# Optimization experiments

Measured on AMD Instinct MI355X. Metric: run time of the kernel, lower is better.

## Reference

```python
import jax, jax.numpy as jnp
import numpy as np

N_WAY = 5
NKPTS = 17
EMBED = 512
N_SUPPORT = 25  # 5-way 5-shot
N_QUERY = 65536


def setup_inputs() -> dict:
    key = jax.random.key(0)
    ks = jax.random.split(key, 12)
    def lin(k, fan_in, fan_out):
        return jax.random.normal(k, (fan_in, fan_out), jnp.float32) / np.float32(np.sqrt(fan_in))
    return {
        'support_features': jax.random.normal(ks[0], (1, N_SUPPORT, EMBED), jnp.float32),
        'support_keypoints': jax.random.uniform(ks[1], (N_SUPPORT, NKPTS, 2), jnp.float32),
        'query_features': jax.random.normal(ks[2], (N_QUERY, EMBED), jnp.float32),
        'image_coords': jax.random.uniform(ks[3], (N_QUERY, 2), jnp.float32) * 512.0,
        'W1': lin(ks[4], EMBED, EMBED), 'b1': jnp.zeros((EMBED,), jnp.float32),
        'W2': lin(ks[5], EMBED, EMBED), 'b2': jnp.zeros((EMBED,), jnp.float32),
        'Wo1': lin(ks[6], EMBED, EMBED // 2), 'bo1': jnp.zeros((EMBED // 2,), jnp.float32),
        'Wo2': lin(ks[7], EMBED // 2, 2), 'bo2': jnp.zeros((2,), jnp.float32),
        'Wc1': lin(ks[8], EMBED, EMBED // 2), 'bc1': jnp.zeros((EMBED // 2,), jnp.float32),
        'Wc2': lin(ks[9], EMBED // 2, 1), 'bc2': jnp.zeros((1,), jnp.float32),
        'temperature': jnp.float32(1.0),
    }


def reference(support_features, support_keypoints, query_features, image_coords,
              W1, b1, W2, b2, Wo1, bo1, Wo2, bo2, Wc1, bc1, Wc2, bc2, temperature):
    eps = 1e-8
    nkpts = support_keypoints.shape[1]
    n_query = query_features.shape[0]
    D = query_features.shape[-1]

    # --- compute_prototypes (batch_size == 1; per-kpt prototype identical by construction) ---
    sf = support_features.reshape(-1, D)                      # [Ns, D]
    h = jnp.maximum(sf @ W1 + b1, 0.0) @ W2 + b2              # prototype_net MLP
    n_per = h.shape[0] // N_WAY
    proto_way = h.reshape(N_WAY, n_per, D).mean(axis=1)       # [n_way, D]
    prototypes = jnp.broadcast_to(proto_way[:, None, :], (N_WAY, nkpts, D))

    # --- compute_distances: 1 - cosine_sim, scaled by temperature ---
    qn = jnp.linalg.norm(query_features, axis=-1)             # [Nq]
    pn = jnp.linalg.norm(proto_way, axis=-1)                  # [n_way]
    sim = (query_features @ proto_way.T) / jnp.maximum(qn[:, None] * pn[None, :], eps)
    dist_way = (1.0 - sim) / temperature                      # [Nq, n_way]
    distances = jnp.broadcast_to(dist_way[:, :, None], (n_query, N_WAY, nkpts))

    # --- predict_keypoints ---
    # avg over kpts is a no-op (identical per kpt); argmin over ways
    class_predictions = jnp.argmin(dist_way, axis=1)          # [Nq] int
    # softmax over a single scalar == 1.0, so keypoints == offset broadcast over kpts
    offset = jnp.maximum(query_features @ Wo1 + bo1, 0.0) @ Wo2 + bo2   # [Nq, 2]
    conf = jax.nn.sigmoid(jnp.maximum(query_features @ Wc1 + bc1, 0.0) @ Wc2 + bc2)  # [Nq, 1]
    keypoints = jnp.broadcast_to(offset[:, None, :], (n_query, nkpts, 2))
    keypoints = jax.nn.sigmoid(keypoints) * image_coords[:, None, :]    # image_coords provided
    confidence = jnp.broadcast_to(conf, (n_query, nkpts))

    return keypoints, confidence, distances, class_predictions, prototypes
```

## Files before the change

kernel.cpp:

```cpp
#include <hip/hip_runtime.h>
#include <hip/hip_bf16.h>

#define NQ 65536
#define DIM 512
#define HID 256
#define NWAY 5
#define NKPTS 17

typedef short bf16x8 __attribute__((ext_vector_type(8)));
typedef float f32x4 __attribute__((ext_vector_type(4)));
typedef _Float16 half8 __attribute__((ext_vector_type(8)));

static __device__ __forceinline__ unsigned short f2bf(float f) {
    unsigned int x = __float_as_uint(f);
    unsigned int r = (x + 0x7fffu + ((x >> 16) & 1u)) >> 16;
    return (unsigned short)r;
}

static __device__ __forceinline__ void async16(void* l, const void* g) {
    __builtin_amdgcn_global_load_lds(
        (const __attribute__((address_space(1))) unsigned int*)g,
        (__attribute__((address_space(3))) unsigned int*)l, 16, 0, 0);
}

__global__ __launch_bounds__(256) void k_sup(const float* __restrict__ sf,
                                             const float* __restrict__ W1, const float* __restrict__ b1,
                                             float* __restrict__ ws_h1) {
    __shared__ float sfl[512];
    __shared__ float red[4][64];
    int bx = blockIdx.x;
    int s = bx >> 3, cb = bx & 7;
    int t = threadIdx.x;
    if (t < 128) ((float4*)sfl)[t] = ((const float4*)(sf + s * DIM))[t];
    __syncthreads();
    int c = cb * 64 + (t & 63);
    int qd = t >> 6;
    const float* Wp = W1 + (size_t)qd * 128 * DIM + c;
    float acc = 0.0f;
    #pragma unroll 4
    for (int kk = 0; kk < 128; kk++)
        acc += sfl[qd * 128 + kk] * Wp[(size_t)kk * DIM];
    red[qd][t & 63] = acc;
    __syncthreads();
    if (t < 64) {
        float h = red[0][t] + red[1][t] + red[2][t] + red[3][t] + b1[cb * 64 + t];
        ws_h1[s * DIM + cb * 64 + t] = fmaxf(h, 0.0f);
    }
}

__global__ __launch_bounds__(256) void k_mid2(const float* __restrict__ ws_h1,
                                              const float* __restrict__ W2, const float* __restrict__ b2,
                                              const float* __restrict__ Wo1, const float* __restrict__ Wc1,
                                              float* __restrict__ ws_proto, unsigned short* __restrict__ wb) {
    int bx = blockIdx.x;
    int t = threadIdx.x;
    if (bx < 40) {
        __shared__ float ml[512];
        __shared__ float red[4][64];
        int w = bx >> 3, cb = bx & 7;
        for (int i = t; i < 512; i += 256) {
            float sum = 0.0f;
            #pragma unroll
            for (int s5 = 0; s5 < 5; s5++) sum += ws_h1[(w * 5 + s5) * DIM + i];
            ml[i] = sum * 0.2f;
        }
        __syncthreads();
        int c = cb * 64 + (t & 63);
        int qd = t >> 6;
        const float* Wp = W2 + (size_t)qd * 128 * DIM + c;
        float acc = 0.0f;
        #pragma unroll 4
        for (int kk = 0; kk < 128; kk++)
            acc += ml[qd * 128 + kk] * Wp[(size_t)kk * DIM];
        red[qd][t & 63] = acc;
        __syncthreads();
        if (t < 64)
            ws_proto[w * DIM + cb * 64 + t] =
                red[0][t] + red[1][t] + red[2][t] + red[3][t] + b2[cb * 64 + t];
    } else {
        __shared__ unsigned short T[64][72];
        int tb = bx - 40;
        const float* src = (tb < 32) ? Wo1 : Wc1;
        int cofs = (tb < 32) ? 0 : 256;
        int tt = tb & 31;
        int kt = tt >> 2;
        int ct = tt & 3;
        int i = t >> 2;
        int qd = t & 3;
        const float* rp = src + (size_t)(kt * 64 + i) * HID + ct * 64 + qd * 16;
        #pragma unroll
        for (int v = 0; v < 4; v++) {
            float4 x = *(const float4*)(rp + v * 4);
            T[qd * 16 + v * 4 + 0][i] = f2bf(x.x);
            T[qd * 16 + v * 4 + 1][i] = f2bf(x.y);
            T[qd * 16 + v * 4 + 2][i] = f2bf(x.z);
            T[qd * 16 + v * 4 + 3][i] = f2bf(x.w);
        }
        __syncthreads();
        int j = t >> 2;
        int part = t & 3;
        uint4 o0 = *(const uint4*)&T[j][part * 16];
        uint4 o1 = *(const uint4*)&T[j][part * 16 + 8];
        unsigned short* dst = wb + (size_t)(cofs + ct * 64 + j) * DIM + kt * 64 + part * 16;
        *(uint4*)dst = o0;
        *(uint4*)(dst + 8) = o1;
    }
}

__global__ __launch_bounds__(256) void k_dist(const float* __restrict__ qf,
                                              const float* __restrict__ ws_proto,
                                              const float* __restrict__ temp_p,
                                              float* __restrict__ out_dist, float* __restrict__ out_class,
                                              float* __restrict__ out_proto) {
    __shared__ float pn_lds[8];
    __shared__ float dlds[64 * NWAY];
    int bx = blockIdx.x, t = threadIdx.x;
    int wv = t >> 6, lane = t & 63;

    if (bx < NWAY * NKPTS && t < 128) {
        f32x4 v = *(const f32x4*)(ws_proto + (bx / NKPTS) * DIM + t * 4);
        *(f32x4*)(out_proto + (size_t)bx * DIM + t * 4) = v;
    }
    for (int w = wv; w < NWAY; w += 4) {
        f32x4 a = *(const f32x4*)(ws_proto + w * DIM + lane * 8);
        f32x4 b = *(const f32x4*)(ws_proto + w * DIM + lane * 8 + 4);
        float ss = a[0]*a[0] + a[1]*a[1] + a[2]*a[2] + a[3]*a[3]
                 + b[0]*b[0] + b[1]*b[1] + b[2]*b[2] + b[3]*b[3];
        #pragma unroll
        for (int off = 32; off > 0; off >>= 1) ss += __shfl_xor(ss, off, 64);
        if (lane == 0) pn_lds[w] = sqrtf(ss);
    }
    float invt = 1.0f / temp_p[0];
    __syncthreads();

    int q = bx * 64 + wv * 16 + (lane & 15);
    int kq = (lane >> 4) * 128;
    const float* qp = qf + (size_t)q * DIM + kq;
    const float* pp = ws_proto + kq;

    float ds[NWAY] = {0, 0, 0, 0, 0};
    float qq = 0.0f;
    #pragma unroll 4
    for (int c = 0; c < 16; c++) {
        f32x4 v0 = *(const f32x4*)(qp + c * 8);
        f32x4 v1 = *(const f32x4*)(qp + c * 8 + 4);
        qq += v0[0]*v0[0] + v0[1]*v0[1] + v0[2]*v0[2] + v0[3]*v0[3]
            + v1[0]*v1[0] + v1[1]*v1[1] + v1[2]*v1[2] + v1[3]*v1[3];
        #pragma unroll
        for (int w = 0; w < NWAY; w++) {
            f32x4 p0 = *(const f32x4*)(pp + w * DIM + c * 8);
            f32x4 p1 = *(const f32x4*)(pp + w * DIM + c * 8 + 4);
            ds[w] += v0[0]*p0[0] + v0[1]*p0[1] + v0[2]*p0[2] + v0[3]*p0[3]
                   + v1[0]*p1[0] + v1[1]*p1[1] + v1[2]*p1[2] + v1[3]*p1[3];
        }
    }
    #pragma unroll
    for (int off = 16; off <= 32; off <<= 1) {
        #pragma unroll
        for (int w = 0; w < NWAY; w++) ds[w] += __shfl_xor(ds[w], off, 64);
        qq += __shfl_xor(qq, off, 64);
    }
    if (lane < 16) {
        float qn = sqrtf(qq);
        float mv = 1e30f; int ami = 0;
        #pragma unroll
        for (int w = 0; w < NWAY; w++) {
            float den = fmaxf(qn * pn_lds[w], 1e-8f);
            float d = (1.0f - ds[w] / den) * invt;
            dlds[(wv * 16 + lane) * NWAY + w] = d;
            if (d < mv) { mv = d; ami = w; }
        }
        out_class[q] = (float)ami;
    }
    __syncthreads();
    int Q0 = bx * 64;
    for (int i = t; i < 64 * NWAY * NKPTS; i += 256) {
        int q2 = i / (NWAY * NKPTS);
        int rem = i - q2 * (NWAY * NKPTS);
        out_dist[(size_t)(Q0 + q2) * (NWAY * NKPTS) + rem] = dlds[q2 * NWAY + rem / NKPTS];
    }
}

__global__ __launch_bounds__(256, 3) void k_gemm(const float* __restrict__ qf,
                                                 const unsigned short* __restrict__ wb,
                                                 const float* __restrict__ bo1, const float* __restrict__ Wo2,
                                                 const float* __restrict__ bo2,
                                                 const float* __restrict__ bc1, const float* __restrict__ Wc2,
                                                 const float* __restrict__ bc2,
                                                 const float* __restrict__ ic,
                                                 float* __restrict__ out_kp, float* __restrict__ out_conf) {
    __shared__ __align__(16) char smem[40960];
    char* Ab = smem;
    char* Bb = smem + 8192;
    _Float16* hl = (_Float16*)smem;
    float* redf = (float*)(smem + 33792);

    int bx = blockIdx.x;
    int mb = bx & 1023, nb = bx >> 10;
    int t = threadIdx.x;
    int wv = t >> 6, lane = t & 63;
    int r = lane & 15, hq = lane >> 4;

    int am = t >> 2, akc = t & 3;
    const float* Ag = qf + ((size_t)mb * 64 + am) * DIM + akc * 8;
    int awoff = am * 64 + ((akc ^ (am & 3) ^ ((am >> 2) & 1)) << 4);

    int srow = lane >> 2;
    int sg = (lane & 3) ^ (srow & 3) ^ ((srow >> 2) & 1);
    const unsigned short* Bg = wb + (size_t)(nb * 256 + wv * 64 + srow) * DIM + sg * 8;

    f32x4 acc[4][4];
    #pragma unroll
    for (int i2 = 0; i2 < 4; i2++)
        #pragma unroll
        for (int j2 = 0; j2 < 4; j2++) { f32x4 z = {0.0f, 0.0f, 0.0f, 0.0f}; acc[i2][j2] = z; }

    float4 aW0 = *(const float4*)(Ag);
    float4 aW1 = *(const float4*)(Ag + 4);
    #pragma unroll
    for (int i = 0; i < 4; i++)
        async16(Bb + wv * 4096 + i * 1024, Bg + (size_t)i * 16 * DIM);
    float4 aN0 = *(const float4*)(Ag + 32);
    float4 aN1 = *(const float4*)(Ag + 36);
    {
        unsigned int p0 = f2bf(aW0.x) | ((unsigned int)f2bf(aW0.y) << 16);
        unsigned int p1 = f2bf(aW0.z) | ((unsigned int)f2bf(aW0.w) << 16);
        unsigned int p2 = f2bf(aW1.x) | ((unsigned int)f2bf(aW1.y) << 16);
        unsigned int p3 = f2bf(aW1.z) | ((unsigned int)f2bf(aW1.w) << 16);
        *(uint4*)(Ab + awoff) = make_uint4(p0, p1, p2, p3);
    }
    aW0 = aN0; aW1 = aN1;
    asm volatile("s_waitcnt lgkmcnt(0) vmcnt(2)" ::: "memory");
    __builtin_amdgcn_s_barrier();
    __builtin_amdgcn_sched_barrier(0);

    int slot8 = (hq ^ (r & 3) ^ ((r >> 2) & 1)) * 8;

    for (int it = 0; it < 15; it++) {
        int par = it & 1;
        #pragma unroll
        for (int i = 0; i < 4; i++)
            async16(Bb + (par ^ 1) * 16384 + wv * 4096 + i * 1024,
                    Bg + (size_t)i * 16 * DIM + (it + 1) * 32);
        float4 aL0, aL1;
        if (it < 14) {
            aL0 = *(const float4*)(Ag + (it + 2) * 32);
            aL1 = *(const float4*)(Ag + (it + 2) * 32 + 4);
        }
        {
            unsigned int p0 = f2bf(aW0.x) | ((unsigned int)f2bf(aW0.y) << 16);
            unsigned int p1 = f2bf(aW0.z) | ((unsigned int)f2bf(aW0.w) << 16);
            unsigned int p2 = f2bf(aW1.x) | ((unsigned int)f2bf(aW1.y) << 16);
            unsigned int p3 = f2bf(aW1.z) | ((unsigned int)f2bf(aW1.w) << 16);
            *(uint4*)(Ab + (par ^ 1) * 4096 + awoff) = make_uint4(p0, p1, p2, p3);
        }
        const unsigned short* Ap = (const unsigned short*)(Ab + par * 4096);
        const unsigned short* Bp = (const unsigned short*)(Bb + par * 16384);
        bf16x8 af[4], bfr[4];
        #pragma unroll
        for (int mt = 0; mt < 4; mt++)
            af[mt] = *(const bf16x8*)(Ap + (mt * 16 + r) * 32 + slot8);
        #pragma unroll
        for (int nt = 0; nt < 4; nt++)
            bfr[nt] = *(const bf16x8*)(Bp + (wv * 64 + nt * 16 + r) * 32 + slot8);
        #pragma unroll
        for (int mt = 0; mt < 4; mt++)
            #pragma unroll
            for (int nt = 0; nt < 4; nt++)
                acc[mt][nt] = __builtin_amdgcn_mfma_f32_16x16x32_bf16(af[mt], bfr[nt], acc[mt][nt], 0, 0, 0);
        if (it < 14) { asm volatile("s_waitcnt lgkmcnt(0) vmcnt(2)" ::: "memory"); }
        else         { asm volatile("s_waitcnt lgkmcnt(0) vmcnt(0)" ::: "memory"); }
        __builtin_amdgcn_s_barrier();
        __builtin_amdgcn_sched_barrier(0);
        if (it < 14) { aW0 = aL0; aW1 = aL1; }
    }
    {
        const unsigned short* Ap = (const unsigned short*)(Ab + 4096);
        const unsigned short* Bp = (const unsigned short*)(Bb + 16384);
        bf16x8 af[4], bfr[4];
        #pragma unroll
        for (int mt = 0; mt < 4; mt++)
            af[mt] = *(const bf16x8*)(Ap + (mt * 16 + r) * 32 + slot8);
        #pragma unroll
        for (int nt = 0; nt < 4; nt++)
            bfr[nt] = *(const bf16x8*)(Bp + (wv * 64 + nt * 16 + r) * 32 + slot8);
        #pragma unroll
        for (int mt = 0; mt < 4; mt++)
            #pragma unroll
            for (int nt = 0; nt < 4; nt++)
                acc[mt][nt] = __builtin_amdgcn_mfma_f32_16x16x32_bf16(af[mt], bfr[nt], acc[mt][nt], 0, 0, 0);
    }
    __syncthreads();

    const float* bias = nb ? bc1 : bo1;
    #pragma unroll
    for (int nt = 0; nt < 4; nt++) {
        int cl = wv * 64 + nt * 16 + r;
        float bv = bias[cl];
        #pragma unroll
        for (int mt = 0; mt < 4; mt++)
            #pragma unroll
            for (int rg = 0; rg < 4; rg++) {
                int ml = mt * 16 + hq * 4 + rg;
                hl[ml * 264 + cl] = (_Float16)fmaxf(acc[mt][nt][rg] + bv, 0.0f);
            }
    }
    __syncthreads();

    int q = t & 63, qt = t >> 6;
    if (nb == 0) {
        float ox = 0.0f, oy = 0.0f;
        #pragma unroll 2
        for (int j0 = 0; j0 < 64; j0 += 8) {
            half8 hv = *(const half8*)(hl + q * 264 + qt * 64 + j0);
            #pragma unroll
            for (int j = 0; j < 8; j++) {
                float2 w2 = *(const float2*)(Wo2 + (qt * 64 + j0 + j) * 2);
                float hf = (float)hv[j];
                ox += hf * w2.x;
                oy += hf * w2.y;
            }
        }
        redf[(qt * 64 + q) * 2] = ox;
        redf[(qt * 64 + q) * 2 + 1] = oy;
        __syncthreads();
        if (t < 64) {
            float sx = bo2[0], sy = bo2[1];
            #pragma unroll
            for (int k2 = 0; k2 < 4; k2++) {
                sx += redf[(k2 * 64 + t) * 2];
                sy += redf[(k2 * 64 + t) * 2 + 1];
            }
            size_t Q = (size_t)mb * 64 + t;
            float2 icv = *(const float2*)(ic + Q * 2);
            float gx = icv.x / (1.0f + __expf(-sx));
            float gy = icv.y / (1.0f + __expf(-sy));
            float2 g2 = make_float2(gx, gy);
            float2* dst = (float2*)(out_kp + Q * 34);
            #pragma unroll
            for (int k2 = 0; k2 < 17; k2++) dst[k2] = g2;
        }
    } else {
        float cs = 0.0f;
        #pragma unroll 2
        for (int j0 = 0; j0 < 64; j0 += 8) {
            half8 hv = *(const half8*)(hl + q * 264 + qt * 64 + j0);
            #pragma unroll
            for (int j = 0; j < 8; j++)
                cs += (float)hv[j] * Wc2[qt * 64 + j0 + j];
        }
        redf[qt * 64 + q] = cs;
        __syncthreads();
        if (t < 64) {
            float s = bc2[0] + redf[t] + redf[64 + t] + redf[128 + t] + redf[192 + t];
            float sg2 = 1.0f / (1.0f + __expf(-s));
            size_t Q = (size_t)mb * 64 + t;
            float* dst = out_conf + Q * 17;
            #pragma unroll
            for (int k2 = 0; k2 < 17; k2++) dst[k2] = sg2;
        }
    }
}

extern "C" void kernel_launch(void* const* d_in, const int* in_sizes, int n_in,
                              void* d_out, int out_size, void* d_ws, size_t ws_size,
                              hipStream_t stream) {
    const float* sf = (const float*)d_in[0];
    const float* qf = (const float*)d_in[2];
    const float* ic = (const float*)d_in[3];
    const float* W1 = (const float*)d_in[4];
    const float* b1 = (const float*)d_in[5];
    const float* W2 = (const float*)d_in[6];
    const float* b2 = (const float*)d_in[7];
    const float* Wo1 = (const float*)d_in[8];
    const float* bo1 = (const float*)d_in[9];
    const float* Wo2 = (const float*)d_in[10];
    const float* bo2 = (const float*)d_in[11];
    const float* Wc1 = (const float*)d_in[12];
    const float* bc1 = (const float*)d_in[13];
    const float* Wc2 = (const float*)d_in[14];
    const float* bc2 = (const float*)d_in[15];
    const float* temp = (const float*)d_in[16];

    float* out = (float*)d_out;
    float* out_kp = out;
    float* out_conf = out + 2228224;
    float* out_dist = out + 3342336;
    float* out_class = out + 8912896;
    float* out_proto = out + 8978432;

    char* ws = (char*)d_ws;
    float* ws_h1 = (float*)ws;
    float* ws_proto = (float*)(ws + 51200);
    unsigned short* ws_wb = (unsigned short*)(ws + 65536);

    hipLaunchKernelGGL(k_sup, dim3(200), dim3(256), 0, stream, sf, W1, b1, ws_h1);
    hipLaunchKernelGGL(k_mid2, dim3(104), dim3(256), 0, stream, ws_h1, W2, b2, Wo1, Wc1, ws_proto, ws_wb);
    hipLaunchKernelGGL(k_dist, dim3(1024), dim3(256), 0, stream, qf, ws_proto, temp,
                       out_dist, out_class, out_proto);
    hipLaunchKernelGGL(k_gemm, dim3(2048), dim3(256), 0, stream, qf, ws_wb,
                       bo1, Wo2, bo2, bc1, Wc2, bc2, ic, out_kp, out_conf);
}
```

Before: 349.3 us.

## Fuse cosine-distance computation into the query GEMM kernel

Removes the separate k_dist kernel. The query-prototype dot products, query norms, argmin class and distance broadcast are now computed inside the GEMM kernel, in the nb==1 blocks, reusing the fp32 A-tile values already loaded for the bf16 conversion. Block indexing is also interleaved so the two N-halves of the same query tile run adjacently, which may improve L2 reuse of query rows. The aim is to avoid re-reading the 128MB query matrix and to save one launch. In exchange it adds LDS use for the prototypes, which may lower occupancy, and extra ALU work on half the blocks, which creates load imbalance.

Measured after the change: 327.7 us. 6.2% less time.

```diff
diff --git a/kernel.cpp b/kernel.cpp
--- a/kernel.cpp
+++ b/kernel.cpp
@@ -107,96 +107,29 @@
     }
 }
 
-__global__ __launch_bounds__(256) void k_dist(const float* __restrict__ qf,
-                                              const float* __restrict__ ws_proto,
-                                              const float* __restrict__ temp_p,
-                                              float* __restrict__ out_dist, float* __restrict__ out_class,
-                                              float* __restrict__ out_proto) {
-    __shared__ float pn_lds[8];
-    __shared__ float dlds[64 * NWAY];
-    int bx = blockIdx.x, t = threadIdx.x;
-    int wv = t >> 6, lane = t & 63;
-
-    if (bx < NWAY * NKPTS && t < 128) {
-        f32x4 v = *(const f32x4*)(ws_proto + (bx / NKPTS) * DIM + t * 4);
-        *(f32x4*)(out_proto + (size_t)bx * DIM + t * 4) = v;
-    }
-    for (int w = wv; w < NWAY; w += 4) {
-        f32x4 a = *(const f32x4*)(ws_proto + w * DIM + lane * 8);
-        f32x4 b = *(const f32x4*)(ws_proto + w * DIM + lane * 8 + 4);
-        float ss = a[0]*a[0] + a[1]*a[1] + a[2]*a[2] + a[3]*a[3]
-                 + b[0]*b[0] + b[1]*b[1] + b[2]*b[2] + b[3]*b[3];
-        #pragma unroll
-        for (int off = 32; off > 0; off >>= 1) ss += __shfl_xor(ss, off, 64);
-        if (lane == 0) pn_lds[w] = sqrtf(ss);
-    }
-    float invt = 1.0f / temp_p[0];
-    __syncthreads();
-
-    int q = bx * 64 + wv * 16 + (lane & 15);
-    int kq = (lane >> 4) * 128;
-    const float* qp = qf + (size_t)q * DIM + kq;
-    const float* pp = ws_proto + kq;
-
-    float ds[NWAY] = {0, 0, 0, 0, 0};
-    float qq = 0.0f;
-    #pragma unroll 4
-    for (int c = 0; c < 16; c++) {
-        f32x4 v0 = *(const f32x4*)(qp + c * 8);
-        f32x4 v1 = *(const f32x4*)(qp + c * 8 + 4);
-        qq += v0[0]*v0[0] + v0[1]*v0[1] + v0[2]*v0[2] + v0[3]*v0[3]
-            + v1[0]*v1[0] + v1[1]*v1[1] + v1[2]*v1[2] + v1[3]*v1[3];
-        #pragma unroll
-        for (int w = 0; w < NWAY; w++) {
-            f32x4 p0 = *(const f32x4*)(pp + w * DIM + c * 8);
-            f32x4 p1 = *(const f32x4*)(pp + w * DIM + c * 8 + 4);
-            ds[w] += v0[0]*p0[0] + v0[1]*p0[1] + v0[2]*p0[2] + v0[3]*p0[3]
-                   + v1[0]*p1[0] + v1[1]*p1[1] + v1[2]*p1[2] + v1[3]*p1[3];
-        }
-    }
-    #pragma unroll
-    for (int off = 16; off <= 32; off <<= 1) {
-        #pragma unroll
-        for (int w = 0; w < NWAY; w++) ds[w] += __shfl_xor(ds[w], off, 64);
-        qq += __shfl_xor(qq, off, 64);
-    }
-    if (lane < 16) {
-        float qn = sqrtf(qq);
-        float mv = 1e30f; int ami = 0;
-        #pragma unroll
-        for (int w = 0; w < NWAY; w++) {
-            float den = fmaxf(qn * pn_lds[w], 1e-8f);
-            float d = (1.0f - ds[w] / den) * invt;
-            dlds[(wv * 16 + lane) * NWAY + w] = d;
-            if (d < mv) { mv = d; ami = w; }
-        }
-        out_class[q] = (float)ami;
-    }
-    __syncthreads();
-    int Q0 = bx * 64;
-    for (int i = t; i < 64 * NWAY * NKPTS; i += 256) {
-        int q2 = i / (NWAY * NKPTS);
-        int rem = i - q2 * (NWAY * NKPTS);
-        out_dist[(size_t)(Q0 + q2) * (NWAY * NKPTS) + rem] = dlds[q2 * NWAY + rem / NKPTS];
-    }
-}
-
-__global__ __launch_bounds__(256, 3) void k_gemm(const float* __restrict__ qf,
-                                                 const unsigned short* __restrict__ wb,
-                                                 const float* __restrict__ bo1, const float* __restrict__ Wo2,
-                                                 const float* __restrict__ bo2,
-                                                 const float* __restrict__ bc1, const float* __restrict__ Wc2,
-                                                 const float* __restrict__ bc2,
-                                                 const float* __restrict__ ic,
-                                                 float* __restrict__ out_kp, float* __restrict__ out_conf) {
-    __shared__ __align__(16) char smem[40960];
+__global__ __launch_bounds__(256, 3) void k_gemm2(const float* __restrict__ qf,
+                                                  const unsigned short* __restrict__ wb,
+                                                  const float* __restrict__ ws_proto,
+                                                  const float* __restrict__ temp_p,
+                                                  const float* __restrict__ bo1, const float* __restrict__ Wo2,
+                                                  const float* __restrict__ bo2,
+                                                  const float* __restrict__ bc1, const float* __restrict__ Wc2,
+                                                  const float* __restrict__ bc2,
+                                                  const float* __restrict__ ic,
+                                                  float* __restrict__ out_kp, float* __restrict__ out_conf,
+                                                  float* __restrict__ out_dist, float* __restrict__ out_class,
+                                                  float* __restrict__ out_proto) {
+    __shared__ __align__(16) char smem[52512];
     char* Ab = smem;
     char* Bb = smem + 8192;
+    float* s_proto = (float*)(smem + 40960);
+    float* pn_lds = (float*)(smem + 51200);
+    float* dlds = (float*)(smem + 51232);
     _Float16* hl = (_Float16*)smem;
     float* redf = (float*)(smem + 33792);
 
     int bx = blockIdx.x;
-    int mb = bx & 1023, nb = bx >> 10;
+    int nb = bx & 1, mb = bx >> 1;
     int t = threadIdx.x;
     int wv = t >> 6, lane = t & 63;
     int r = lane & 15, hq = lane >> 4;
@@ -214,6 +147,18 @@
     for (int i2 = 0; i2 < 4; i2++)
         #pragma unroll
         for (int j2 = 0; j2 < 4; j2++) { f32x4 z = {0.0f, 0.0f, 0.0f, 0.0f}; acc[i2][j2] = z; }
+    float ds[NWAY] = {0, 0, 0, 0, 0};
+    float qq = 0.0f;
+    float invt = 0.0f;
+
+    if (nb) {
+        for (int i = t; i < NWAY * DIM; i += 256) s_proto[i] = ws_proto[i];
+        if (mb < NWAY * NKPTS && t < 128) {
+            f32x4 v = *(const f32x4*)(ws_proto + (mb / NKPTS) * DIM + t * 4);
+            *(f32x4*)(out_proto + (size_t)mb * DIM + t * 4) = v;
+        }
+        invt = 1.0f / temp_p[0];
+    }
 
     float4 aW0 = *(const float4*)(Ag);
     float4 aW1 = *(const float4*)(Ag + 4);
@@ -229,10 +174,25 @@
         unsigned int p3 = f2bf(aW1.z) | ((unsigned int)f2bf(aW1.w) << 16);
         *(uint4*)(Ab + awoff) = make_uint4(p0, p1, p2, p3);
     }
+    float4 c0 = aW0, c1 = aW1;
     aW0 = aN0; aW1 = aN1;
     asm volatile("s_waitcnt lgkmcnt(0) vmcnt(2)" ::: "memory");
     __builtin_amdgcn_s_barrier();
     __builtin_amdgcn_sched_barrier(0);
+
+    if (nb) {
+        float av[8] = {c0.x, c0.y, c0.z, c0.w, c1.x, c1.y, c1.z, c1.w};
+        int kb = akc * 8;
+        #pragma unroll
+        for (int w = 0; w < NWAY; w++) {
+            f32x4 pv0 = *(const f32x4*)(s_proto + w * DIM + kb);
+            f32x4 pv1 = *(const f32x4*)(s_proto + w * DIM + kb + 4);
+            ds[w] += av[0] * pv0[0] + av[1] * pv0[1] + av[2] * pv0[2] + av[3] * pv0[3]
+                   + av[4] * pv1[0] + av[5] * pv1[1] + av[6] * pv1[2] + av[7] * pv1[3];
+        }
+        #pragma unroll
+        for (int j = 0; j < 8; j++) qq += av[j] * av[j];
+    }
 
     int slot8 = (hq ^ (r & 3) ^ ((r >> 2) & 1)) * 8;
 
@@ -254,6 +214,19 @@
             unsigned int p3 = f2bf(aW1.z) | ((unsigned int)f2bf(aW1.w) << 16);
             *(uint4*)(Ab + (par ^ 1) * 4096 + awoff) = make_uint4(p0, p1, p2, p3);
         }
+        if (nb) {
+            float av[8] = {aW0.x, aW0.y, aW0.z, aW0.w, aW1.x, aW1.y, aW1.z, aW1.w};
+            int kb = (it + 1) * 32 + akc * 8;
+            #pragma unroll
+            for (int w = 0; w < NWAY; w++) {
+                f32x4 pv0 = *(const f32x4*)(s_proto + w * DIM + kb);
+                f32x4 pv1 = *(const f32x4*)(s_proto + w * DIM + kb + 4);
+                ds[w] += av[0] * pv0[0] + av[1] * pv0[1] + av[2] * pv0[2] + av[3] * pv0[3]
+                       + av[4] * pv1[0] + av[5] * pv1[1] + av[6] * pv1[2] + av[7] * pv1[3];
+            }
+            #pragma unroll
+            for (int j = 0; j < 8; j++) qq += av[j] * av[j];
+        }
         const unsigned short* Ap = (const unsigned short*)(Ab + par * 4096);
         const unsigned short* Bp = (const unsigned short*)(Bb + par * 16384);
         bf16x8 af[4], bfr[4];
@@ -291,6 +264,18 @@
                 acc[mt][nt] = __builtin_amdgcn_mfma_f32_16x16x32_bf16(af[mt], bfr[nt], acc[mt][nt], 0, 0, 0);
     }
     __syncthreads();
+
+    if (nb) {
+        for (int w = wv; w < NWAY; w += 4) {
+            f32x4 a = *(const f32x4*)(s_proto + w * DIM + lane * 8);
+            f32x4 b = *(const f32x4*)(s_proto + w * DIM + lane * 8 + 4);
+            float ss = a[0]*a[0] + a[1]*a[1] + a[2]*a[2] + a[3]*a[3]
+                     + b[0]*b[0] + b[1]*b[1] + b[2]*b[2] + b[3]*b[3];
+            #pragma unroll
+            for (int off = 32; off > 0; off >>= 1) ss += __shfl_xor(ss, off, 64);
+            if (lane == 0) pn_lds[w] = sqrtf(ss);
+        }
+    }
 
     const float* bias = nb ? bc1 : bo1;
     #pragma unroll
@@ -341,6 +326,24 @@
             for (int k2 = 0; k2 < 17; k2++) dst[k2] = g2;
         }
     } else {
+        #pragma unroll
+        for (int off = 1; off <= 2; off <<= 1) {
+            #pragma unroll
+            for (int w = 0; w < NWAY; w++) ds[w] += __shfl_xor(ds[w], off, 64);
+            qq += __shfl_xor(qq, off, 64);
+        }
+        if (akc == 0) {
+            float qn = sqrtf(qq);
+            float mv = 1e30f; int ami = 0;
+            #pragma unroll
+            for (int w = 0; w < NWAY; w++) {
+                float den = fmaxf(qn * pn_lds[w], 1e-8f);
+                float d = (1.0f - ds[w] / den) * invt;
+                dlds[am * 5 + w] = d;
+                if (d < mv) { mv = d; ami = w; }
+            }
+            out_class[mb * 64 + am] = (float)ami;
+        }
         float cs = 0.0f;
         #pragma unroll 2
         for (int j0 = 0; j0 < 64; j0 += 8) {
@@ -358,6 +361,11 @@
             float* dst = out_conf + Q * 17;
             #pragma unroll
             for (int k2 = 0; k2 < 17; k2++) dst[k2] = sg2;
+        }
+        for (int i = t; i < 64 * NWAY * NKPTS; i += 256) {
+            int q2 = i / (NWAY * NKPTS);
+            int rem = i - q2 * (NWAY * NKPTS);
+            out_dist[(size_t)(mb * 64 + q2) * (NWAY * NKPTS) + rem] = dlds[q2 * 5 + rem / NKPTS];
         }
     }
 }
@@ -396,8 +404,7 @@
 
     hipLaunchKernelGGL(k_sup, dim3(200), dim3(256), 0, stream, sf, W1, b1, ws_h1);
     hipLaunchKernelGGL(k_mid2, dim3(104), dim3(256), 0, stream, ws_h1, W2, b2, Wo1, Wc1, ws_proto, ws_wb);
-    hipLaunchKernelGGL(k_dist, dim3(1024), dim3(256), 0, stream, qf, ws_proto, temp,
+    hipLaunchKernelGGL(k_gemm2, dim3(2048), dim3(256), 0, stream, qf, ws_wb, ws_proto, temp,
+                       bo1, Wo2, bo2, bc1, Wc2, bc2, ic, out_kp, out_conf,
                        out_dist, out_class, out_proto);
-    hipLaunchKernelGGL(k_gemm, dim3(2048), dim3(256), 0, stream, qf, ws_wb,
-                       bo1, Wo2, bo2, bc1, Wc2, bc2, ic, out_kp, out_conf);
-}
+}
```
